# Kernel optimization log

Hardware: AMD Instinct MI355X
Metric: run time of the kernel (lower is better)

Reference implementation:

```python
import jax, jax.numpy as jnp
import numpy as np

NHEAD = 8
DC = 32
IN_CHS = 2 * NHEAD  # cross_coverage and self_coverage both True
EPS = 1e-5  # BatchNorm1d default eps


def conv2d(x, w, pad):
    return jax.lax.conv_general_dilated(
        x, w, window_strides=(1, 1), padding=[(pad, pad), (pad, pad)],
        dimension_numbers=('NCHW', 'OIHW', 'NCHW'))


def setup_inputs() -> dict:
    key = jax.random.key(0)
    ks = jax.random.split(key, 10)
    b, t, H, W = 8, 256, 16, 32
    l = H * W
    prev_attn = jax.random.uniform(ks[0], (b * NHEAD, t, l), dtype=jnp.float32)
    curr_attn = jax.random.uniform(ks[1], (b * NHEAD, t, l), dtype=jnp.float32)
    key_padding_mask = jax.random.uniform(ks[2], (b, l)) < 0.25  # True = padded
    conv_w = jax.random.normal(ks[3], (DC, IN_CHS, 5, 5), jnp.float32) * 0.05
    conv_b = jnp.zeros((DC,), jnp.float32)
    proj_w = jax.random.normal(ks[4], (NHEAD, DC, 1, 1), jnp.float32) * 0.05
    g_w1 = jax.random.normal(ks[5], (IN_CHS // 2, IN_CHS, 3, 3), jnp.float32) * 0.05
    g_b1 = jnp.zeros((IN_CHS // 2,), jnp.float32)
    g_w2 = jax.random.normal(ks[6], (IN_CHS, IN_CHS // 2, 1, 1), jnp.float32) * 0.05
    g_b2 = jnp.zeros((IN_CHS,), jnp.float32)
    bn_gamma = jnp.ones((NHEAD,), jnp.float32)
    bn_beta = jnp.zeros((NHEAD,), jnp.float32)
    return dict(prev_attn=prev_attn, key_padding_mask=key_padding_mask, h=H,
                curr_attn=curr_attn, tgt_vocab=113,
                conv_w=conv_w, conv_b=conv_b, proj_w=proj_w,
                g_w1=g_w1, g_b1=g_b1, g_w2=g_w2, g_b2=g_b2,
                bn_gamma=bn_gamma, bn_beta=bn_beta)


def reference(prev_attn, key_padding_mask, h, curr_attn, tgt_vocab,
              conv_w, conv_b, proj_w, g_w1, g_b1, g_w2, g_b2, bn_gamma, bn_beta):
    n = NHEAD
    b = prev_attn.shape[0] // n
    t = curr_attn.shape[1]
    l = key_padding_mask.shape[1]
    w = l // h

    prev = prev_attn.reshape(b, n, t, l)
    curr = curr_attn.reshape(b, n, t, l)
    attns = jnp.concatenate([prev, curr], axis=1)  # [b, 2n, t, l]
    c = attns.shape[1]

    # gating network on per-step attention images: [(b t), c, h, w]
    attns_bt = attns.transpose(0, 2, 1, 3).reshape(b * t, c, h, w)
    g = jax.nn.relu(conv2d(attns_bt, g_w1, 1) + g_b1[None, :, None, None])
    g = g.mean(axis=(2, 3))  # AdaptiveAvgPool2d((1,1)) -> [(b t), c//2]
    g = jax.nn.sigmoid(jnp.einsum('bi,oi->bo', g, g_w2[:, :, 0, 0]) + g_b2)
    gate = g.reshape(b, t, c).transpose(0, 2, 1)[..., None]  # [b, c, t, 1]

    gated = attns * gate
    cum = jnp.cumsum(gated, axis=2) - gated  # exclusive cumulative coverage
    cum2d = cum.transpose(0, 2, 1, 3).reshape(b * t, c, h, w)

    mask = jnp.broadcast_to(key_padding_mask.reshape(b, 1, 1, h, w),
                            (b, t, 1, h, w)).reshape(b * t, 1, h, w)

    cov = jax.nn.relu(conv2d(cum2d, conv_w, 2) + conv_b[None, :, None, None])
    cov = jnp.where(mask, 0.0, cov)
    cov = jnp.einsum('bdhw,nd->bnhw', cov, proj_w[:, :, 0, 0])  # 1x1 proj, no bias

    # MaskBatchNorm2d: BN statistics over non-masked positions only
    nm = (~mask).astype(cov.dtype)  # [(b t), 1, h, w]
    cnt = nm.sum()
    mean = (cov * nm).sum(axis=(0, 2, 3), keepdims=True) / cnt  # per-channel
    var = (jnp.square(cov - mean) * nm).sum(axis=(0, 2, 3), keepdims=True) / cnt
    xn = (cov - mean) * jax.lax.rsqrt(var + EPS) * bn_gamma[None, :, None, None] \
        + bn_beta[None, :, None, None]
    cov = jnp.where(mask, cov, xn)  # masked positions keep pre-BN values (zeros)

    out = cov.reshape(b, t, n, l).transpose(0, 2, 1, 3).reshape(b * n, t, l)
    return out
```

## Files before the change

kernel.cpp:

```cpp
#include <hip/hip_runtime.h>
#include <hip/hip_bf16.h>

#define BB   8
#define TT   256
#define NH   8
#define CC   16
#define HH   16
#define WW   32
#define LL   512
#define DCH  32
#define GC   8

typedef __attribute__((ext_vector_type(8))) short s8b;
typedef __attribute__((ext_vector_type(4))) float f32x4;

__device__ __forceinline__ ushort f2bfu(float v) {
  __hip_bfloat16 h = __float2bfloat16(v);
  ushort s;
  __builtin_memcpy(&s, &h, 2);
  return s;
}
__device__ __forceinline__ float bf2f(ushort u) {
  unsigned w = ((unsigned)u) << 16;
  float f;
  __builtin_memcpy(&f, &w, 4);
  return f;
}

__global__ __launch_bounds__(256) void k_gen(const float* __restrict__ cw,
                                             const float* __restrict__ pw,
                                             const float* __restrict__ gw1,
                                             ushort* __restrict__ bfrag,
                                             ushort* __restrict__ pwf,
                                             ushort* __restrict__ bfragG) {
  int idx = blockIdx.x * 256 + threadIdx.x;
  if (idx < 13312) {
    int j = idx & 7, lane = (idx >> 3) & 63, nt = (idx >> 9) & 1, s = idx >> 10;
    int quad = lane >> 4, col = lane & 15;
    int k = s * 32 + quad * 8 + j;
    int n = nt * 16 + col;
    float v = (k < 400) ? cw[(n * CC + (k & 15)) * 25 + (k >> 4)] : 0.f;
    bfrag[idx] = f2bfu(v);
  } else if (idx < 13824) {
    int i2 = idx - 13312;
    int j = i2 & 7, lane = i2 >> 3;
    int quad = lane >> 4, col = lane & 15;
    float v = (col < NH) ? pw[col * DCH + quad * 8 + j] : 0.f;
    pwf[i2] = f2bfu(v);
  } else if (idx < 16384) {
    int i3 = idx - 13824;
    int j = i3 & 7, lane = (i3 >> 3) & 63, s = i3 >> 9;
    int quad = lane >> 4, col = lane & 15;
    int k = s * 32 + quad * 8 + j;
    float v = 0.f;
    if (k < 144 && col < GC) v = gw1[(col * CC + (k & 15)) * 9 + (k >> 4)];
    bfragG[i3] = f2bfu(v);
  }
}

__global__ __launch_bounds__(256) void k_gate(
    const float* __restrict__ prev, const float* __restrict__ curr,
    const ushort* __restrict__ bfragG, const float* __restrict__ gb1,
    const float* __restrict__ gw2, const float* __restrict__ gb2,
    ushort* __restrict__ gated) {
  __shared__ __align__(16) ushort img[8 * 1728];
  __shared__ float redg[64];
  __shared__ float pooled[16];
  __shared__ float gateS[16];

  int tid = threadIdx.x;
  int lane = tid & 63, w = tid >> 6;
  int bt = blockIdx.x;
  int b = bt >> 8, t = bt & 255;
  int quad = lane >> 4, col = lane & 15;
  int qh = quad >> 1, icb = (quad & 1) * 8;

  for (int i = tid; i < 1728; i += 256) ((uint4*)img)[i] = (uint4){0, 0, 0, 0};
  __syncthreads();

#pragma unroll
  for (int it = 0; it < 4; ++it) {
#pragma unroll
    for (int e = 0; e < 2; ++e) {
      int W = ((it * 4 + w) * 2 + e) * 64 + lane;
      int cp = W >> 8, pp = W & 255;
      int l0 = pp * 2;
      const float* src = (cp < 4) ? prev : curr;
      int chb = (cp & 3) * 2;
      const float* p0 = src + ((size_t)(b * NH + chb) * TT + t) * LL + l0;
      float2 fa = *(const float2*)p0;
      float2 fb = *(const float2*)(p0 + TT * LL);
      unsigned lo = (unsigned)f2bfu(fa.x) | ((unsigned)f2bfu(fb.x) << 16);
      unsigned hi = (unsigned)f2bfu(fa.y) | ((unsigned)f2bfu(fb.y) << 16);
      int r = l0 >> 5, x = l0 & 31;
      int slot = (r + 1) * 48 + 8 + x;
      *(uint2*)&img[cp * 1728 + slot * 2] = (uint2){lo, hi};
    }
  }
  __syncthreads();

  f32x4 acc[8];
#pragma unroll
  for (int mi = 0; mi < 8; ++mi) acc[mi] = (f32x4){0.f, 0.f, 0.f, 0.f};
  int mtbase = w * 8;
  int ab[8];
#pragma unroll
  for (int mi = 0; mi < 8; ++mi) {
    int mt = mtbase + mi;
    int py = mt >> 1, px = ((mt & 1) << 4) + col;
    ab[mi] = (icb >> 1) * 1728 + (py * 48 + 7 + px) * 2;
  }
  const int offE[5] = {0, 2, 49, 96, 98};
  const int offO[5] = {1, 48, 50, 97, 98};
  const s8b* bG = (const s8b*)bfragG;
#pragma unroll
  for (int s = 0; s < 5; ++s) {
    s8b bf = bG[s * 64 + lane];
    int off2 = (qh ? offO[s] : offE[s]) * 2;
#pragma unroll
    for (int mi = 0; mi < 8; ++mi) {
      union { unsigned u[4]; s8b v; } A;
      int a0 = ab[mi] + off2;
#pragma unroll
      for (int p = 0; p < 4; ++p) A.u[p] = *(const unsigned*)&img[a0 + p * 1728];
      acc[mi] = __builtin_amdgcn_mfma_f32_16x16x32_bf16(A.v, bf, acc[mi], 0, 0, 0);
    }
  }

  float gb1c = (col < GC) ? gb1[col] : 0.f;
  float s = 0.f;
#pragma unroll
  for (int mi = 0; mi < 8; ++mi)
#pragma unroll
    for (int r = 0; r < 4; ++r) s += fmaxf(acc[mi][r] + gb1c, 0.f);
  s += __shfl_down(s, 16, 64);
  s += __shfl_down(s, 32, 64);
  if (lane < 16) redg[w * 16 + lane] = s;
  __syncthreads();
  if (tid < 16)
    pooled[tid] = (redg[tid] + redg[16 + tid] + redg[32 + tid] + redg[48 + tid]) *
                  (1.0f / (float)LL);
  __syncthreads();
  if (tid < 16) {
    float z = gb2[tid];
#pragma unroll
    for (int i = 0; i < GC; ++i) z = fmaf(pooled[i], gw2[tid * GC + i], z);
    gateS[tid] = 1.f / (1.f + __expf(-z));
  }
  __syncthreads();

#pragma unroll
  for (int it = 0; it < 4; ++it) {
    int c = it * 4 + w;
    float g = gateS[c];
    const float* src = (c < NH) ? prev : curr;
    const float* p0 = src + ((size_t)(b * NH + (c & 7)) * TT + t) * LL + lane * 8;
    float4 v0 = *(const float4*)p0;
    float4 v1 = *(const float4*)(p0 + 4);
    ushort u[8];
    u[0] = f2bfu(v0.x * g); u[1] = f2bfu(v0.y * g);
    u[2] = f2bfu(v0.z * g); u[3] = f2bfu(v0.w * g);
    u[4] = f2bfu(v1.x * g); u[5] = f2bfu(v1.y * g);
    u[6] = f2bfu(v1.z * g); u[7] = f2bfu(v1.w * g);
    uint4 ov;
    __builtin_memcpy(&ov, u, 16);
    *(uint4*)(gated + ((size_t)(b * CC + c) * TT + t) * LL + lane * 8) = ov;
  }
}

__global__ __launch_bounds__(256) void k_cumA(const ushort* __restrict__ gated,
                                              float* __restrict__ csum) {
  int idx = blockIdx.x * 256 + threadIdx.x;
  int l = idx & 511, tc = (idx >> 9) & 7, c = (idx >> 12) & 15, b = idx >> 16;
  const ushort* g = gated + ((size_t)(b * CC + c) * TT + tc * 32) * LL + l;
  float s = 0.f;
#pragma unroll 8
  for (int j = 0; j < 32; ++j) s += bf2f(g[j * LL]);
  csum[((b * CC + c) * 8 + tc) * LL + l] = s;
}

__global__ __launch_bounds__(256) void k_cumB(ushort* __restrict__ gated,
                                              const float* __restrict__ csum) {
  int idx = blockIdx.x * 256 + threadIdx.x;
  int l = idx & 511, tc = (idx >> 9) & 7, c = (idx >> 12) & 15, b = idx >> 16;
  float run = 0.f;
  const float* cs = csum + ((b * CC + c) * 8) * LL + l;
  for (int u = 0; u < tc; ++u) run += cs[u * LL];
  ushort* g = gated + ((size_t)(b * CC + c) * TT + tc * 32) * LL + l;
#pragma unroll 4
  for (int j = 0; j < 32; ++j) {
    ushort raw = g[j * LL];
    float v = bf2f(raw);
    g[j * LL] = f2bfu(run);
    run += v;
  }
}

__global__ __launch_bounds__(256, 2) void k_cov(
    const ushort* __restrict__ cum, const ushort* __restrict__ bfrag,
    const ushort* __restrict__ pwf, const float* __restrict__ cb,
    const int* __restrict__ mask, float* __restrict__ out,
    float* __restrict__ sums) {
  __shared__ __align__(16) ushort img[8 * 1920];
  __shared__ __align__(16) ushort scr[4 * 576];
  __shared__ float redp[128];
  __shared__ float redc[4];

  int tid = threadIdx.x;
  int lane = tid & 63, w = tid >> 6;
  int bt = blockIdx.x;
  int b = bt >> 8, t = bt & 255;
  int quad = lane >> 4, col = lane & 15;
  int qh = quad >> 1, icb = (quad & 1) * 8;

  for (int i = tid; i < 1920; i += 256) ((uint4*)img)[i] = (uint4){0, 0, 0, 0};
  __syncthreads();

#pragma unroll
  for (int it = 0; it < 4; ++it) {
#pragma unroll
    for (int e = 0; e < 2; ++e) {
      int W = ((it * 4 + w) * 2 + e) * 64 + lane;
      int cp = W >> 8, pp = W & 255;
      int l0 = pp * 2;
      const ushort* p0 = cum + ((size_t)(b * CC + cp * 2) * TT + t) * LL + l0;
      unsigned a = *(const unsigned*)p0;
      unsigned bb2 = *(const unsigned*)(p0 + TT * LL);
      unsigned lo = (a & 0xFFFFu) | (bb2 << 16);
      unsigned hi = (a >> 16) | (bb2 & 0xFFFF0000u);
      int r = l0 >> 5, x = l0 & 31;
      int slot = (r + 2) * 48 + 8 + x;
      *(uint2*)&img[cp * 1920 + slot * 2] = (uint2){lo, hi};
    }
  }
  __syncthreads();

  f32x4 acc[8][2];
#pragma unroll
  for (int mi = 0; mi < 8; ++mi) {
    acc[mi][0] = (f32x4){0.f, 0.f, 0.f, 0.f};
    acc[mi][1] = (f32x4){0.f, 0.f, 0.f, 0.f};
  }
  int mtbase = w * 8;
  int ab[8];
#pragma unroll
  for (int mi = 0; mi < 8; ++mi) {
    int mt = mtbase + mi;
    int py = mt >> 1, px = ((mt & 1) << 4) + col;
    ab[mi] = (icb >> 1) * 1920 + (py * 48 + 6 + px) * 2;
  }
  const int offE[13] = {0, 2, 4, 49, 51, 96, 98, 100, 145, 147, 192, 194, 196};
  const int offO[13] = {1, 3, 48, 50, 52, 97, 99, 144, 146, 148, 193, 195, 196};
  const s8b* bfr = (const s8b*)bfrag;
#pragma unroll
  for (int s = 0; s < 13; ++s) {
    s8b bf0 = bfr[(s * 2) * 64 + lane];
    s8b bf1 = bfr[(s * 2 + 1) * 64 + lane];
    int off2 = (qh ? offO[s] : offE[s]) * 2;
#pragma unroll
    for (int mi = 0; mi < 8; ++mi) {
      union { unsigned u[4]; s8b v; } A;
      int a0 = ab[mi] + off2;
#pragma unroll
      for (int p = 0; p < 4; ++p) A.u[p] = *(const unsigned*)&img[a0 + p * 1920];
      acc[mi][0] = __builtin_amdgcn_mfma_f32_16x16x32_bf16(A.v, bf0, acc[mi][0], 0, 0, 0);
      acc[mi][1] = __builtin_amdgcn_mfma_f32_16x16x32_bf16(A.v, bf1, acc[mi][1], 0, 0, 0);
    }
  }

  int wb = w * 576;
  float cb0 = cb[col], cb1 = cb[col + 16];
  s8b pf = ((const s8b*)pwf)[lane];
  float psum = 0.f, psq = 0.f, pcnt = 0.f;
  float* outbase = out + ((size_t)(b * NH + col) * TT + t) * LL;
  const int* mrow = mask + b * LL;
#pragma unroll
  for (int mi = 0; mi < 8; ++mi) {
    int mt = mtbase + mi;
#pragma unroll
    for (int r = 0; r < 4; ++r) {
      int p = quad * 4 + r;
      scr[wb + col * 18 + p] = f2bfu(fmaxf(acc[mi][0][r] + cb0, 0.f));
      scr[wb + (col + 16) * 18 + p] = f2bfu(fmaxf(acc[mi][1][r] + cb1, 0.f));
    }
    ushort u[8];
#pragma unroll
    for (int e = 0; e < 8; ++e) u[e] = scr[wb + (quad * 8 + e) * 18 + col];
    s8b a2;
    __builtin_memcpy(&a2, u, 16);
    f32x4 zero = {0.f, 0.f, 0.f, 0.f};
    f32x4 d2 = __builtin_amdgcn_mfma_f32_16x16x32_bf16(a2, pf, zero, 0, 0, 0);
    int4 m4 = *(const int4*)(mrow + mt * 16 + quad * 4);
    float k0 = m4.x ? 0.f : 1.f;
    float k1 = m4.y ? 0.f : 1.f;
    float k2 = m4.z ? 0.f : 1.f;
    float k3 = m4.w ? 0.f : 1.f;
    if (col < NH) {
      float* op = outbase + mt * 16 + quad * 4;
      float v0 = d2[0] * k0; op[0] = v0; psum += v0; psq += v0 * v0;
      float v1 = d2[1] * k1; op[1] = v1; psum += v1; psq += v1 * v1;
      float v2 = d2[2] * k2; op[2] = v2; psum += v2; psq += v2 * v2;
      float v3 = d2[3] * k3; op[3] = v3; psum += v3; psq += v3 * v3;
    }
    if (col == 0) pcnt += k0 + k1 + k2 + k3;
  }

  psum += __shfl_down(psum, 16, 64); psum += __shfl_down(psum, 32, 64);
  psq  += __shfl_down(psq, 16, 64);  psq  += __shfl_down(psq, 32, 64);
  pcnt += __shfl_down(pcnt, 16, 64); pcnt += __shfl_down(pcnt, 32, 64);
  if (lane < 16) {
    redp[(w * 16 + lane) * 2] = psum;
    redp[(w * 16 + lane) * 2 + 1] = psq;
    if (lane == 0) redc[w] = pcnt;
  }
  __syncthreads();
  if (tid < 17) {
    float v;
    if (tid < 8) {
      v = redp[tid * 2] + redp[(16 + tid) * 2] + redp[(32 + tid) * 2] + redp[(48 + tid) * 2];
    } else if (tid < 16) {
      int nh = tid - 8;
      v = redp[nh * 2 + 1] + redp[(16 + nh) * 2 + 1] + redp[(32 + nh) * 2 + 1] + redp[(48 + nh) * 2 + 1];
    } else {
      v = redc[0] + redc[1] + redc[2] + redc[3];
    }
    atomicAdd(&sums[tid], v);
  }
}

__global__ __launch_bounds__(256) void k_bn(
    float* __restrict__ out, const float* __restrict__ sums,
    const int* __restrict__ mask, const float* __restrict__ gamma,
    const float* __restrict__ beta) {
  __shared__ float sc[NH], sh[NH];
  int tid = threadIdx.x;
  if (tid < NH) {
    float cnt = sums[16];
    float mean = sums[tid] / cnt;
    float var = sums[NH + tid] / cnt - mean * mean;
    float inv = rsqrtf(var + 1e-5f) * gamma[tid];
    sc[tid] = inv;
    sh[tid] = fmaf(-mean, inv, beta[tid]);
  }
  __syncthreads();
  size_t e = ((size_t)blockIdx.x * 256 + tid) * 4;
  int l = (int)(e & (LL - 1));
  int bn = (int)(e >> 17);
  int n = bn & 7, b = bn >> 3;
  const int4 mv = *(const int4*)(mask + b * LL + l);
  float4 v = *(float4*)(out + e);
  float s = sc[n], h = sh[n];
  v.x = mv.x ? v.x : fmaf(v.x, s, h);
  v.y = mv.y ? v.y : fmaf(v.y, s, h);
  v.z = mv.z ? v.z : fmaf(v.z, s, h);
  v.w = mv.w ? v.w : fmaf(v.w, s, h);
  *(float4*)(out + e) = v;
}

extern "C" void kernel_launch(void* const* d_in, const int* in_sizes, int n_in,
                              void* d_out, int out_size, void* d_ws, size_t ws_size,
                              hipStream_t stream) {
  const float* prev   = (const float*)d_in[0];
  const int*   mask   = (const int*)d_in[1];
  const float* curr   = (const float*)d_in[3];
  const float* conv_w = (const float*)d_in[5];
  const float* conv_b = (const float*)d_in[6];
  const float* proj_w = (const float*)d_in[7];
  const float* g_w1   = (const float*)d_in[8];
  const float* g_b1   = (const float*)d_in[9];
  const float* g_w2   = (const float*)d_in[10];
  const float* g_b2   = (const float*)d_in[11];
  const float* bn_g   = (const float*)d_in[12];
  const float* bn_b   = (const float*)d_in[13];
  float* out = (float*)d_out;

  char* ws = (char*)d_ws;
  ushort* bfrag  = (ushort*)(ws);
  ushort* pwf    = (ushort*)(ws + 26624);
  ushort* bfragG = (ushort*)(ws + 27648);
  float*  sums   = (float*)(ws + 32768);
  ushort* gated  = (ushort*)(ws + 65536);
  float*  csum   = (float*)(ws + 65536 + 33554432);

  hipMemsetAsync(sums, 0, 17 * sizeof(float), stream);
  k_gen<<<64, 256, 0, stream>>>(conv_w, proj_w, g_w1, bfrag, pwf, bfragG);
  k_gate<<<BB * TT, 256, 0, stream>>>(prev, curr, bfragG, g_b1, g_w2, g_b2, gated);
  k_cumA<<<2048, 256, 0, stream>>>(gated, csum);
  k_cumB<<<2048, 256, 0, stream>>>(gated, csum);
  k_cov<<<BB * TT, 256, 0, stream>>>(gated, bfrag, pwf, conv_b, mask, out, sums);
  k_bn<<<(BB * NH * TT * LL) / (256 * 4), 256, 0, stream>>>(out, sums, mask, bn_g, bn_b);
}
```

Measured before the change: 223.0 us.

## Stop materializing gated tensor; apply gate inside cumsum kernels and pad LDS strides

The gate kernel now writes only per-(b,c,t) sigmoid gate scalars instead of a full bf16 gated tensor. Both cumsum passes read the fp32 attention inputs directly and multiply by the gate, and the second pass writes the exclusive cumsum to a separate buffer. This removes the gated write and re-reads, but the scan kernels now read fp32 inputs (twice the bytes of bf16). It also pads the LDS image and scratch strides and packs the scratch stores into 8-byte writes to reduce bank conflicts, and folds the sums memset into k_gen.

```diff
diff --git a/kernel.cpp b/kernel.cpp
--- a/kernel.cpp
+++ b/kernel.cpp
@@ -11,6 +11,9 @@
 #define DCH  32
 #define GC   8
 
+#define PSC  1928
+#define PSG  1736
+
 typedef __attribute__((ext_vector_type(8))) short s8b;
 typedef __attribute__((ext_vector_type(4))) float f32x4;
 
@@ -20,20 +23,16 @@
   __builtin_memcpy(&s, &h, 2);
   return s;
 }
-__device__ __forceinline__ float bf2f(ushort u) {
-  unsigned w = ((unsigned)u) << 16;
-  float f;
-  __builtin_memcpy(&f, &w, 4);
-  return f;
-}
 
 __global__ __launch_bounds__(256) void k_gen(const float* __restrict__ cw,
                                              const float* __restrict__ pw,
                                              const float* __restrict__ gw1,
                                              ushort* __restrict__ bfrag,
                                              ushort* __restrict__ pwf,
-                                             ushort* __restrict__ bfragG) {
+                                             ushort* __restrict__ bfragG,
+                                             float* __restrict__ sums) {
   int idx = blockIdx.x * 256 + threadIdx.x;
+  if (idx < 17) sums[idx] = 0.f;
   if (idx < 13312) {
     int j = idx & 7, lane = (idx >> 3) & 63, nt = (idx >> 9) & 1, s = idx >> 10;
     int quad = lane >> 4, col = lane & 15;
@@ -62,11 +61,10 @@
     const float* __restrict__ prev, const float* __restrict__ curr,
     const ushort* __restrict__ bfragG, const float* __restrict__ gb1,
     const float* __restrict__ gw2, const float* __restrict__ gb2,
-    ushort* __restrict__ gated) {
-  __shared__ __align__(16) ushort img[8 * 1728];
+    float* __restrict__ gate2) {
+  __shared__ __align__(16) ushort img[8 * PSG];
   __shared__ float redg[64];
   __shared__ float pooled[16];
-  __shared__ float gateS[16];
 
   int tid = threadIdx.x;
   int lane = tid & 63, w = tid >> 6;
@@ -75,7 +73,7 @@
   int quad = lane >> 4, col = lane & 15;
   int qh = quad >> 1, icb = (quad & 1) * 8;
 
-  for (int i = tid; i < 1728; i += 256) ((uint4*)img)[i] = (uint4){0, 0, 0, 0};
+  for (int i = tid; i < PSG; i += 256) ((uint4*)img)[i] = (uint4){0, 0, 0, 0};
   __syncthreads();
 
 #pragma unroll
@@ -94,7 +92,7 @@
       unsigned hi = (unsigned)f2bfu(fa.y) | ((unsigned)f2bfu(fb.y) << 16);
       int r = l0 >> 5, x = l0 & 31;
       int slot = (r + 1) * 48 + 8 + x;
-      *(uint2*)&img[cp * 1728 + slot * 2] = (uint2){lo, hi};
+      *(uint2*)&img[cp * PSG + slot * 2] = (uint2){lo, hi};
     }
   }
   __syncthreads();
@@ -108,7 +106,7 @@
   for (int mi = 0; mi < 8; ++mi) {
     int mt = mtbase + mi;
     int py = mt >> 1, px = ((mt & 1) << 4) + col;
-    ab[mi] = (icb >> 1) * 1728 + (py * 48 + 7 + px) * 2;
+    ab[mi] = (icb >> 1) * PSG + (py * 48 + 7 + px) * 2;
   }
   const int offE[5] = {0, 2, 49, 96, 98};
   const int offO[5] = {1, 48, 50, 97, 98};
@@ -122,7 +120,7 @@
       union { unsigned u[4]; s8b v; } A;
       int a0 = ab[mi] + off2;
 #pragma unroll
-      for (int p = 0; p < 4; ++p) A.u[p] = *(const unsigned*)&img[a0 + p * 1728];
+      for (int p = 0; p < 4; ++p) A.u[p] = *(const unsigned*)&img[a0 + p * PSG];
       acc[mi] = __builtin_amdgcn_mfma_f32_16x16x32_bf16(A.v, bf, acc[mi], 0, 0, 0);
     }
   }
@@ -145,54 +143,43 @@
     float z = gb2[tid];
 #pragma unroll
     for (int i = 0; i < GC; ++i) z = fmaf(pooled[i], gw2[tid * GC + i], z);
-    gateS[tid] = 1.f / (1.f + __expf(-z));
-  }
-  __syncthreads();
-
-#pragma unroll
-  for (int it = 0; it < 4; ++it) {
-    int c = it * 4 + w;
-    float g = gateS[c];
-    const float* src = (c < NH) ? prev : curr;
-    const float* p0 = src + ((size_t)(b * NH + (c & 7)) * TT + t) * LL + lane * 8;
-    float4 v0 = *(const float4*)p0;
-    float4 v1 = *(const float4*)(p0 + 4);
-    ushort u[8];
-    u[0] = f2bfu(v0.x * g); u[1] = f2bfu(v0.y * g);
-    u[2] = f2bfu(v0.z * g); u[3] = f2bfu(v0.w * g);
-    u[4] = f2bfu(v1.x * g); u[5] = f2bfu(v1.y * g);
-    u[6] = f2bfu(v1.z * g); u[7] = f2bfu(v1.w * g);
-    uint4 ov;
-    __builtin_memcpy(&ov, u, 16);
-    *(uint4*)(gated + ((size_t)(b * CC + c) * TT + t) * LL + lane * 8) = ov;
-  }
-}
-
-__global__ __launch_bounds__(256) void k_cumA(const ushort* __restrict__ gated,
+    gate2[(b * CC + tid) * TT + t] = 1.f / (1.f + __expf(-z));
+  }
+}
+
+__global__ __launch_bounds__(256) void k_cumA(const float* __restrict__ prev,
+                                              const float* __restrict__ curr,
+                                              const float* __restrict__ gate2,
                                               float* __restrict__ csum) {
   int idx = blockIdx.x * 256 + threadIdx.x;
   int l = idx & 511, tc = (idx >> 9) & 7, c = (idx >> 12) & 15, b = idx >> 16;
-  const ushort* g = gated + ((size_t)(b * CC + c) * TT + tc * 32) * LL + l;
+  const float* src = (c < NH) ? prev : curr;
+  const float* a = src + ((size_t)(b * NH + (c & 7)) * TT + tc * 32) * LL + l;
+  const float* g = gate2 + (b * CC + c) * TT + tc * 32;
   float s = 0.f;
 #pragma unroll 8
-  for (int j = 0; j < 32; ++j) s += bf2f(g[j * LL]);
+  for (int j = 0; j < 32; ++j) s = fmaf(a[(size_t)j * LL], g[j], s);
   csum[((b * CC + c) * 8 + tc) * LL + l] = s;
 }
 
-__global__ __launch_bounds__(256) void k_cumB(ushort* __restrict__ gated,
-                                              const float* __restrict__ csum) {
+__global__ __launch_bounds__(256) void k_cumB(const float* __restrict__ prev,
+                                              const float* __restrict__ curr,
+                                              const float* __restrict__ gate2,
+                                              const float* __restrict__ csum,
+                                              ushort* __restrict__ cum) {
   int idx = blockIdx.x * 256 + threadIdx.x;
   int l = idx & 511, tc = (idx >> 9) & 7, c = (idx >> 12) & 15, b = idx >> 16;
   float run = 0.f;
   const float* cs = csum + ((b * CC + c) * 8) * LL + l;
   for (int u = 0; u < tc; ++u) run += cs[u * LL];
-  ushort* g = gated + ((size_t)(b * CC + c) * TT + tc * 32) * LL + l;
+  const float* src = (c < NH) ? prev : curr;
+  const float* a = src + ((size_t)(b * NH + (c & 7)) * TT + tc * 32) * LL + l;
+  const float* g = gate2 + (b * CC + c) * TT + tc * 32;
+  ushort* o = cum + ((size_t)(b * CC + c) * TT + tc * 32) * LL + l;
 #pragma unroll 4
   for (int j = 0; j < 32; ++j) {
-    ushort raw = g[j * LL];
-    float v = bf2f(raw);
-    g[j * LL] = f2bfu(run);
-    run += v;
+    o[(size_t)j * LL] = f2bfu(run);
+    run = fmaf(a[(size_t)j * LL], g[j], run);
   }
 }
 
@@ -201,8 +188,8 @@
     const ushort* __restrict__ pwf, const float* __restrict__ cb,
     const int* __restrict__ mask, float* __restrict__ out,
     float* __restrict__ sums) {
-  __shared__ __align__(16) ushort img[8 * 1920];
-  __shared__ __align__(16) ushort scr[4 * 576];
+  __shared__ __align__(16) ushort img[8 * PSC];
+  __shared__ __align__(16) ushort scr[4 * 640];
   __shared__ float redp[128];
   __shared__ float redc[4];
 
@@ -213,7 +200,7 @@
   int quad = lane >> 4, col = lane & 15;
   int qh = quad >> 1, icb = (quad & 1) * 8;
 
-  for (int i = tid; i < 1920; i += 256) ((uint4*)img)[i] = (uint4){0, 0, 0, 0};
+  for (int i = tid; i < PSC; i += 256) ((uint4*)img)[i] = (uint4){0, 0, 0, 0};
   __syncthreads();
 
 #pragma unroll
@@ -230,7 +217,7 @@
       unsigned hi = (a >> 16) | (bb2 & 0xFFFF0000u);
       int r = l0 >> 5, x = l0 & 31;
       int slot = (r + 2) * 48 + 8 + x;
-      *(uint2*)&img[cp * 1920 + slot * 2] = (uint2){lo, hi};
+      *(uint2*)&img[cp * PSC + slot * 2] = (uint2){lo, hi};
     }
   }
   __syncthreads();
@@ -247,7 +234,7 @@
   for (int mi = 0; mi < 8; ++mi) {
     int mt = mtbase + mi;
     int py = mt >> 1, px = ((mt & 1) << 4) + col;
-    ab[mi] = (icb >> 1) * 1920 + (py * 48 + 6 + px) * 2;
+    ab[mi] = (icb >> 1) * PSC + (py * 48 + 6 + px) * 2;
   }
   const int offE[13] = {0, 2, 4, 49, 51, 96, 98, 100, 145, 147, 192, 194, 196};
   const int offO[13] = {1, 3, 48, 50, 52, 97, 99, 144, 146, 148, 193, 195, 196};
@@ -262,13 +249,13 @@
       union { unsigned u[4]; s8b v; } A;
       int a0 = ab[mi] + off2;
 #pragma unroll
-      for (int p = 0; p < 4; ++p) A.u[p] = *(const unsigned*)&img[a0 + p * 1920];
+      for (int p = 0; p < 4; ++p) A.u[p] = *(const unsigned*)&img[a0 + p * PSC];
       acc[mi][0] = __builtin_amdgcn_mfma_f32_16x16x32_bf16(A.v, bf0, acc[mi][0], 0, 0, 0);
       acc[mi][1] = __builtin_amdgcn_mfma_f32_16x16x32_bf16(A.v, bf1, acc[mi][1], 0, 0, 0);
     }
   }
 
-  int wb = w * 576;
+  int wb = w * 640;
   float cb0 = cb[col], cb1 = cb[col + 16];
   s8b pf = ((const s8b*)pwf)[lane];
   float psum = 0.f, psq = 0.f, pcnt = 0.f;
@@ -277,15 +264,20 @@
 #pragma unroll
   for (int mi = 0; mi < 8; ++mi) {
     int mt = mtbase + mi;
+    ushort w0[4], w1[4];
 #pragma unroll
     for (int r = 0; r < 4; ++r) {
-      int p = quad * 4 + r;
-      scr[wb + col * 18 + p] = f2bfu(fmaxf(acc[mi][0][r] + cb0, 0.f));
-      scr[wb + (col + 16) * 18 + p] = f2bfu(fmaxf(acc[mi][1][r] + cb1, 0.f));
-    }
+      w0[r] = f2bfu(fmaxf(acc[mi][0][r] + cb0, 0.f));
+      w1[r] = f2bfu(fmaxf(acc[mi][1][r] + cb1, 0.f));
+    }
+    uint2 pk0, pk1;
+    __builtin_memcpy(&pk0, w0, 8);
+    __builtin_memcpy(&pk1, w1, 8);
+    *(uint2*)&scr[wb + col * 20 + quad * 4] = pk0;
+    *(uint2*)&scr[wb + (col + 16) * 20 + quad * 4] = pk1;
     ushort u[8];
 #pragma unroll
-    for (int e = 0; e < 8; ++e) u[e] = scr[wb + (quad * 8 + e) * 18 + col];
+    for (int e = 0; e < 8; ++e) u[e] = scr[wb + (quad * 8 + e) * 20 + col];
     s8b a2;
     __builtin_memcpy(&a2, u, 16);
     f32x4 zero = {0.f, 0.f, 0.f, 0.f};
@@ -379,14 +371,14 @@
   ushort* pwf    = (ushort*)(ws + 26624);
   ushort* bfragG = (ushort*)(ws + 27648);
   float*  sums   = (float*)(ws + 32768);
-  ushort* gated  = (ushort*)(ws + 65536);
-  float*  csum   = (float*)(ws + 65536 + 33554432);
-
-  hipMemsetAsync(sums, 0, 17 * sizeof(float), stream);
-  k_gen<<<64, 256, 0, stream>>>(conv_w, proj_w, g_w1, bfrag, pwf, bfragG);
-  k_gate<<<BB * TT, 256, 0, stream>>>(prev, curr, bfragG, g_b1, g_w2, g_b2, gated);
-  k_cumA<<<2048, 256, 0, stream>>>(gated, csum);
-  k_cumB<<<2048, 256, 0, stream>>>(gated, csum);
-  k_cov<<<BB * TT, 256, 0, stream>>>(gated, bfrag, pwf, conv_b, mask, out, sums);
+  float*  gate2  = (float*)(ws + 36864);
+  ushort* cum    = (ushort*)(ws + 36864 + 131072);
+  float*  csum   = (float*)(ws + 36864 + 131072 + 33554432);
+
+  k_gen<<<64, 256, 0, stream>>>(conv_w, proj_w, g_w1, bfrag, pwf, bfragG, sums);
+  k_gate<<<BB * TT, 256, 0, stream>>>(prev, curr, bfragG, g_b1, g_w2, g_b2, gate2);
+  k_cumA<<<2048, 256, 0, stream>>>(prev, curr, gate2, csum);
+  k_cumB<<<2048, 256, 0, stream>>>(prev, curr, gate2, csum, cum);
+  k_cov<<<BB * TT, 256, 0, stream>>>(cum, bfrag, pwf, conv_b, mask, out, sums);
   k_bn<<<(BB * NH * TT * LL) / (256 * 4), 256, 0, stream>>>(out, sums, mask, bn_g, bn_b);
 }
```

Result: faster. 216.7 us (-2.8%).
